# Kernel optimization log

Measured on AMD Instinct MI355X. Metric: run time of the kernel, lower is better.

## Reference

```python
import jax, jax.numpy as jnp
import numpy as np

DIM = 512
NUM_HEADS = 8
HEAD_DIM = DIM // NUM_HEADS
B, S = 2, 2048


def setup_inputs() -> dict:
    key = jax.random.key(0)
    ks = jax.random.split(key, 16)
    scale = 1.0 / np.sqrt(DIM)
    inp = {
        "x": jax.random.normal(ks[0], (B, S, DIM), dtype=jnp.float32),
        "Qexpl": jax.random.normal(ks[1], (B, S, DIM), dtype=jnp.float32),
        "Kexpl": jax.random.normal(ks[2], (B, S, DIM), dtype=jnp.float32),
        "fl": jax.random.uniform(ks[3], (B,), dtype=jnp.float32),
        "fu": jax.random.uniform(ks[4], (B,), dtype=jnp.float32),
        "age": jax.random.uniform(ks[5], (B,), dtype=jnp.float32),
        "gender": jax.random.uniform(ks[6], (B,), dtype=jnp.float32),
        # Linear params: weight stored as [out, in] like torch; y = x @ W.T + b
        "Wq": jax.random.normal(ks[7], (DIM, DIM), dtype=jnp.float32) * scale,
        "bq": jnp.zeros((DIM,), dtype=jnp.float32),
        "Wk": jax.random.normal(ks[8], (DIM, DIM), dtype=jnp.float32) * scale,
        "bk": jnp.zeros((DIM,), dtype=jnp.float32),
        "Wv": jax.random.normal(ks[9], (DIM, DIM), dtype=jnp.float32) * scale,
        "bv": jnp.zeros((DIM,), dtype=jnp.float32),
        "Wo": jax.random.normal(ks[10], (DIM, DIM), dtype=jnp.float32) * scale,
        "bo": jnp.zeros((DIM,), dtype=jnp.float32),
    }
    return inp


def reference(x, Qexpl, Kexpl, fl, fu, age, gender, Wq, bq, Wk, bk, Wv, bv, Wo, bo):
    # drofe_fn is None -> Q/K projections used directly.
    Q = Qexpl @ Wq.T + bq            # [B, S, D]
    K = Kexpl @ Wk.T + bk            # [B, S, D]
    V = x @ Wv.T + bv                # [B, S, D]

    def split_heads(t):  # [B, S, D] -> [B, H, S, hd]
        return t.reshape(B, S, NUM_HEADS, HEAD_DIM).transpose(0, 2, 1, 3)

    Qh, Kh, Vh = split_heads(Q), split_heads(K), split_heads(V)
    scale = 1.0 / np.sqrt(HEAD_DIM).astype(np.float32)
    scores = jnp.einsum("bhqd,bhkd->bhqk", Qh, Kh) * scale  # [B, H, S, S]
    weights = jax.nn.softmax(scores, axis=-1)
    attn = jnp.einsum("bhqk,bhkd->bhqd", weights, Vh)        # [B, H, S, hd]
    attn = attn.transpose(0, 2, 1, 3).reshape(B, S, DIM)
    return attn @ Wo.T + bo
```

## Files before the change

### kernel.cpp

```cpp
#include <hip/hip_runtime.h>
#include <hip/hip_bf16.h>

typedef unsigned short ushort_t;
typedef __attribute__((ext_vector_type(8))) short bf16x8;
typedef __attribute__((ext_vector_type(4))) float f32x4;

__device__ __forceinline__ ushort_t f2bf(float f) {
    union { float f; unsigned u; } v; v.f = f;
    unsigned r = v.u + 0x7FFF + ((v.u >> 16) & 1);
    return (ushort_t)(r >> 16);
}
__device__ __forceinline__ bf16x8 ld8(const ushort_t* p) { return *(const bf16x8*)p; }

__device__ __forceinline__ unsigned cvt2(float x, float y) {
    __hip_bfloat162 h = __float22bfloat162_rn(make_float2(x, y));
    unsigned r; __builtin_memcpy(&r, &h, 4); return r;
}
__device__ __forceinline__ bf16x8 pack8f(float4 a, float4 b) {
    union { unsigned u[4]; bf16x8 v; } o;
    o.u[0] = cvt2(a.x, a.y); o.u[1] = cvt2(a.z, a.w);
    o.u[2] = cvt2(b.x, b.y); o.u[3] = cvt2(b.z, b.w);
    return o.v;
}

__global__ __launch_bounds__(256, 2)
void proj_qkv_kernel(const float* __restrict__ Qe, const float* __restrict__ Ke,
                     const float* __restrict__ x,
                     const float* __restrict__ Wq, const float* __restrict__ Wk,
                     const float* __restrict__ Wv,
                     const float* __restrict__ bq, const float* __restrict__ bk,
                     const float* __restrict__ bv,
                     ushort_t* __restrict__ Qo, ushort_t* __restrict__ Ko,
                     ushort_t* __restrict__ Vt)
{
    __shared__ ushort_t smem[2 * 128 * 72];
    ushort_t* lA = smem;
    ushort_t* lB = smem + 128 * 72;

    const int z = blockIdx.z;
    const float* A = (z == 0) ? Qe : (z == 1) ? Ke : x;
    const float* W = (z == 0) ? Wq : (z == 1) ? Wk : Wv;
    const float* bias = (z == 0) ? bq : (z == 1) ? bk : bv;

    const int m0 = blockIdx.y * 128, n0 = blockIdx.x * 128;
    const int t = threadIdx.x;
    const int lane = t & 63, wave = t >> 6;
    const int wm = (wave & 1) * 64, wn = (wave >> 1) * 64;
    const int fr = lane & 15, quad = lane >> 4;

    f32x4 acc[4][4] = {};
    float4 fa[4][2], fw[4][2];

#pragma unroll
    for (int i = 0; i < 4; ++i) {
        int s = i * 256 + t;
        int r = s >> 3, jp = s & 7;
        const float* pa = A + (size_t)(m0 + r) * 512 + jp * 8;
        fa[i][0] = *(const float4*)pa; fa[i][1] = *(const float4*)(pa + 4);
        const float* pw = W + (size_t)(n0 + r) * 512 + jp * 8;
        fw[i][0] = *(const float4*)pw; fw[i][1] = *(const float4*)(pw + 4);
    }

    for (int kk = 0; kk < 8; ++kk) {
        if (kk) __syncthreads();
#pragma unroll
        for (int i = 0; i < 4; ++i) {
            int s = i * 256 + t;
            int r = s >> 3, jp = s & 7;
            *(bf16x8*)(lA + r * 72 + jp * 8) = pack8f(fa[i][0], fa[i][1]);
            *(bf16x8*)(lB + r * 72 + jp * 8) = pack8f(fw[i][0], fw[i][1]);
        }
        __syncthreads();
        if (kk < 7) {
            int k0 = (kk + 1) * 64;
#pragma unroll
            for (int i = 0; i < 4; ++i) {
                int s = i * 256 + t;
                int r = s >> 3, jp = s & 7;
                const float* pa = A + (size_t)(m0 + r) * 512 + k0 + jp * 8;
                fa[i][0] = *(const float4*)pa; fa[i][1] = *(const float4*)(pa + 4);
                const float* pw = W + (size_t)(n0 + r) * 512 + k0 + jp * 8;
                fw[i][0] = *(const float4*)pw; fw[i][1] = *(const float4*)(pw + 4);
            }
        }

#pragma unroll
        for (int ks = 0; ks < 2; ++ks) {
            bf16x8 af[4], bfrag[4];
#pragma unroll
            for (int mt = 0; mt < 4; ++mt)
                af[mt] = ld8(lA + (wm + mt * 16 + fr) * 72 + (ks * 4 + quad) * 8);
#pragma unroll
            for (int nt = 0; nt < 4; ++nt)
                bfrag[nt] = ld8(lB + (wn + nt * 16 + fr) * 72 + (ks * 4 + quad) * 8);
#pragma unroll
            for (int mt = 0; mt < 4; ++mt)
#pragma unroll
                for (int nt = 0; nt < 4; ++nt)
                    acc[mt][nt] = __builtin_amdgcn_mfma_f32_16x16x32_bf16(
                        af[mt], bfrag[nt], acc[mt][nt], 0, 0, 0);
        }
    }

    const float C1 = 0.125f * 1.44269504088896340736f;
    if (z != 2) {
        ushort_t* dst = (z == 0) ? Qo : Ko;
#pragma unroll
        for (int nt = 0; nt < 4; ++nt) {
            int n = n0 + wn + nt * 16 + fr;
            float bb = bias[n];
#pragma unroll
            for (int mt = 0; mt < 4; ++mt) {
                int mb = m0 + wm + mt * 16 + quad * 4;
                if (z == 0) {
#pragma unroll
                    for (int r = 0; r < 4; ++r)
                        dst[(size_t)(mb + r) * 512 + n] = f2bf((acc[mt][nt][r] + bb) * C1);
                } else {
#pragma unroll
                    for (int r = 0; r < 4; ++r)
                        dst[(size_t)(mb + r) * 512 + n] = f2bf(acc[mt][nt][r] + bb);
                }
            }
        }
    } else {
        __syncthreads();
        ushort_t* lT = smem;
#pragma unroll
        for (int nt = 0; nt < 4; ++nt) {
            int nl = wn + nt * 16 + fr;
            float bb = bias[n0 + nl];
#pragma unroll
            for (int mt = 0; mt < 4; ++mt) {
                int tm = wm + mt * 16 + quad * 4;
#pragma unroll
                for (int r = 0; r < 4; ++r) {
                    int tl = tm + r;
                    int sg = 8 * (tl & 15) + ((tl >> 4) & 7);
                    lT[nl * 136 + sg] = f2bf(acc[mt][nt][r] + bb);
                }
            }
        }
        __syncthreads();
        const int bidx = m0 >> 11, m0t = m0 & 2047;
#pragma unroll
        for (int i = 0; i < 8; ++i) {
            int s = i * 256 + t;
            int row = s >> 4, c = s & 15;
            int n = n0 + row;
            int h = n >> 6, d = n & 63;
            bf16x8 v = ld8(lT + row * 136 + c * 8);
            *(bf16x8*)(Vt + ((size_t)((bidx * 8 + h) * 64 + d)) * 2048 + m0t + c * 8) = v;
        }
    }
}

__global__ __launch_bounds__(256, 2)
void gemm_o_kernel(const ushort_t* __restrict__ A, const float* __restrict__ W,
                   const float* __restrict__ bias, float* __restrict__ dst)
{
    __shared__ ushort_t lA[64 * 72];
    __shared__ ushort_t lB[64 * 72];
    const int m0 = blockIdx.y * 64, n0 = blockIdx.x * 64;
    const int t = threadIdx.x;
    const int lane = t & 63, wave = t >> 6;
    const int wm = (wave & 1) * 32, wn = (wave >> 1) * 32;
    const int fr = lane & 15, quad = lane >> 4;

    f32x4 acc[2][2] = {};
    bf16x8 va[2];
    float4 fw[2][2];

#pragma unroll
    for (int i = 0; i < 2; ++i) {
        int s = i * 256 + t;
        int r = s >> 3, jp = s & 7;
        va[i] = ld8(A + (size_t)(m0 + r) * 512 + jp * 8);
        const float* p = W + (size_t)(n0 + r) * 512 + jp * 8;
        fw[i][0] = *(const float4*)p; fw[i][1] = *(const float4*)(p + 4);
    }

    for (int kk = 0; kk < 8; ++kk) {
        if (kk) __syncthreads();
#pragma unroll
        for (int i = 0; i < 2; ++i) {
            int s = i * 256 + t;
            int r = s >> 3, jp = s & 7;
            *(bf16x8*)(lA + r * 72 + jp * 8) = va[i];
            *(bf16x8*)(lB + r * 72 + jp * 8) = pack8f(fw[i][0], fw[i][1]);
        }
        __syncthreads();
        if (kk < 7) {
            int k0 = (kk + 1) * 64;
#pragma unroll
            for (int i = 0; i < 2; ++i) {
                int s = i * 256 + t;
                int r = s >> 3, jp = s & 7;
                va[i] = ld8(A + (size_t)(m0 + r) * 512 + k0 + jp * 8);
                const float* p = W + (size_t)(n0 + r) * 512 + k0 + jp * 8;
                fw[i][0] = *(const float4*)p; fw[i][1] = *(const float4*)(p + 4);
            }
        }

        bf16x8 af[2][2], bfrag[2][2];
#pragma unroll
        for (int ks = 0; ks < 2; ++ks) {
#pragma unroll
            for (int mt = 0; mt < 2; ++mt)
                af[mt][ks] = ld8(lA + (wm + mt * 16 + fr) * 72 + (ks * 4 + quad) * 8);
#pragma unroll
            for (int nt = 0; nt < 2; ++nt)
                bfrag[nt][ks] = ld8(lB + (wn + nt * 16 + fr) * 72 + (ks * 4 + quad) * 8);
        }
#pragma unroll
        for (int ks = 0; ks < 2; ++ks)
#pragma unroll
            for (int mt = 0; mt < 2; ++mt)
#pragma unroll
                for (int nt = 0; nt < 2; ++nt)
                    acc[mt][nt] = __builtin_amdgcn_mfma_f32_16x16x32_bf16(
                        af[mt][ks], bfrag[nt][ks], acc[mt][nt], 0, 0, 0);
    }

#pragma unroll
    for (int nt = 0; nt < 2; ++nt) {
        int n = n0 + wn + nt * 16 + fr;
        float bb = bias[n];
#pragma unroll
        for (int mt = 0; mt < 2; ++mt) {
            int mb = m0 + wm + mt * 16 + quad * 4;
#pragma unroll
            for (int r = 0; r < 4; ++r)
                dst[(size_t)(mb + r) * 512 + n] = acc[mt][nt][r] + bb;
        }
    }
}

__global__ __launch_bounds__(256, 2)
void attn_kernel(const ushort_t* __restrict__ Q, const ushort_t* __restrict__ K,
                 const ushort_t* __restrict__ Vt, ushort_t* __restrict__ O)
{
    __shared__ ushort_t lK[128 * 72];
    __shared__ ushort_t lVt[64 * 136];
    __shared__ ushort_t lP[64 * 136];

    const int b = blockIdx.z, h = blockIdx.y;
    const int q0 = blockIdx.x * 64;
    const int t = threadIdx.x;
    const int lane = t & 63, wave = t >> 6;
    const int wq = wave * 16;
    const int fr = lane & 15, quad = lane >> 4;

    bf16x8 aq[2];
    {
        const ushort_t* qp = Q + (size_t)(b * 2048 + q0 + wq + fr) * 512 + h * 64 + quad * 8;
        aq[0] = ld8(qp);
        aq[1] = ld8(qp + 32);
    }

    f32x4 oacc[4] = {};
    float lpart[4] = {};
    bf16x8 vk[4], vv[4];

#pragma unroll
    for (int i = 0; i < 4; ++i) {
        int s = i * 256 + t;
        int r = s >> 3, jp = s & 7;
        vk[i] = ld8(K + (size_t)(b * 2048 + r) * 512 + h * 64 + jp * 8);
        int r2 = s >> 4, jp2 = s & 15;
        vv[i] = ld8(Vt + (size_t)((b * 8 + h) * 64 + r2) * 2048 + jp2 * 8);
    }

    for (int kv = 0; kv < 2048; kv += 128) {
        if (kv) __syncthreads();
#pragma unroll
        for (int i = 0; i < 4; ++i) {
            int s = i * 256 + t;
            int r = s >> 3, jp = s & 7;
            *(bf16x8*)(lK + r * 72 + jp * 8) = vk[i];
            int r2 = s >> 4, jp2 = s & 15;
            *(bf16x8*)(lVt + r2 * 136 + jp2 * 8) = vv[i];
        }
        __syncthreads();
        if (kv + 128 < 2048) {
            int kn = kv + 128;
#pragma unroll
            for (int i = 0; i < 4; ++i) {
                int s = i * 256 + t;
                int r = s >> 3, jp = s & 7;
                vk[i] = ld8(K + (size_t)(b * 2048 + kn + r) * 512 + h * 64 + jp * 8);
                int r2 = s >> 4, jp2 = s & 15;
                vv[i] = ld8(Vt + (size_t)((b * 8 + h) * 64 + r2) * 2048 + kn + jp2 * 8);
            }
        }

        f32x4 sc[8] = {};
#pragma unroll
        for (int ks = 0; ks < 2; ++ks)
#pragma unroll
            for (int nt = 0; nt < 8; ++nt) {
                bf16x8 kb = ld8(lK + (nt * 16 + fr) * 72 + (ks * 4 + quad) * 8);
                sc[nt] = __builtin_amdgcn_mfma_f32_16x16x32_bf16(aq[ks], kb, sc[nt], 0, 0, 0);
            }

#pragma unroll
        for (int r = 0; r < 4; ++r) {
            int row = wq + quad * 4 + r;
            float pv[8];
            float acc = 0.f;
#pragma unroll
            for (int nt = 0; nt < 8; ++nt) {
                pv[nt] = exp2f(sc[nt][r]);
                acc += pv[nt];
            }
            lpart[r] += acc;
            union { unsigned u[4]; bf16x8 v; } pu;
            pu.u[0] = cvt2(pv[0], pv[1]); pu.u[1] = cvt2(pv[2], pv[3]);
            pu.u[2] = cvt2(pv[4], pv[5]); pu.u[3] = cvt2(pv[6], pv[7]);
            *(bf16x8*)(lP + row * 136 + fr * 8) = pu.v;
        }

#pragma unroll
        for (int ks = 0; ks < 4; ++ks) {
            bf16x8 ap = ld8(lP + (wq + fr) * 136 + ks * 32 + quad * 8);
#pragma unroll
            for (int nt = 0; nt < 4; ++nt) {
                bf16x8 vb = ld8(lVt + (nt * 16 + fr) * 136 + ks * 32 + quad * 8);
                oacc[nt] = __builtin_amdgcn_mfma_f32_16x16x32_bf16(ap, vb, oacc[nt], 0, 0, 0);
            }
        }
    }

#pragma unroll
    for (int r = 0; r < 4; ++r) {
        float rs = lpart[r];
#pragma unroll
        for (int o = 1; o < 16; o <<= 1)
            rs += __shfl_xor(rs, o, 64);
        float inv = 1.f / rs;
        int q = q0 + wq + quad * 4 + r;
#pragma unroll
        for (int nt = 0; nt < 4; ++nt) {
            int d = nt * 16 + fr;
            O[(size_t)(b * 2048 + q) * 512 + h * 64 + d] = f2bf(oacc[nt][r] * inv);
        }
    }
}

extern "C" void kernel_launch(void* const* d_in, const int* in_sizes, int n_in,
                              void* d_out, int out_size, void* d_ws, size_t ws_size,
                              hipStream_t stream) {
    const float* x   = (const float*)d_in[0];
    const float* Qe  = (const float*)d_in[1];
    const float* Ke  = (const float*)d_in[2];
    const float* Wq  = (const float*)d_in[7];
    const float* bq  = (const float*)d_in[8];
    const float* Wk  = (const float*)d_in[9];
    const float* bk  = (const float*)d_in[10];
    const float* Wv  = (const float*)d_in[11];
    const float* bv  = (const float*)d_in[12];
    const float* Wo  = (const float*)d_in[13];
    const float* bo  = (const float*)d_in[14];

    const size_t NTOK = 2 * 2048;
    const size_t ACT = NTOK * 512;

    ushort_t* p = (ushort_t*)d_ws;
    ushort_t* Qws = p; p += ACT;
    ushort_t* Kws = p; p += ACT;
    ushort_t* Vt  = p; p += ACT;
    ushort_t* Ows = p; p += ACT;

    proj_qkv_kernel<<<dim3(4, 32, 3), 256, 0, stream>>>(Qe, Ke, x, Wq, Wk, Wv,
                                                        bq, bk, bv, Qws, Kws, Vt);
    attn_kernel<<<dim3(32, 8, 2), 256, 0, stream>>>(Qws, Kws, Vt, Ows);
    gemm_o_kernel<<<dim3(8, 64), 256, 0, stream>>>(Ows, Wo, bo, (float*)d_out);
}
```

Before: 167.0 us.

## Restructure attention with direct global-to-LDS loads, double-buffered K, and swizzled LDS

Rewrites the attention kernel to use 2 waves per block, each owning 32 query rows, which doubles register reuse of each K/V fragment across two MFMA tiles. K and V tiles move straight from global memory into LDS with global_load_lds. K is double-buffered so the next tile's load overlaps the current compute. Padded LDS rows are replaced by XOR swizzling to avoid bank conflicts. The cost is fewer waves per block and reliance on manual vmcnt waits, which lowers occupancy and latency hiding.

```diff
diff --git a/kernel.cpp b/kernel.cpp
--- a/kernel.cpp
+++ b/kernel.cpp
@@ -21,6 +21,12 @@
     o.u[0] = cvt2(a.x, a.y); o.u[1] = cvt2(a.z, a.w);
     o.u[2] = cvt2(b.x, b.y); o.u[3] = cvt2(b.z, b.w);
     return o.v;
+}
+
+__device__ __forceinline__ void gload_lds16(const ushort_t* g, ushort_t* l) {
+    __builtin_amdgcn_global_load_lds(
+        (const __attribute__((address_space(1))) void*)g,
+        (__attribute__((address_space(3))) void*)l, 16, 0, 0);
 }
 
 __global__ __launch_bounds__(256, 2)
@@ -236,115 +242,121 @@
     }
 }
 
-__global__ __launch_bounds__(256, 2)
+__global__ __launch_bounds__(128, 1)
 void attn_kernel(const ushort_t* __restrict__ Q, const ushort_t* __restrict__ K,
                  const ushort_t* __restrict__ Vt, ushort_t* __restrict__ O)
 {
-    __shared__ ushort_t lK[128 * 72];
-    __shared__ ushort_t lVt[64 * 136];
-    __shared__ ushort_t lP[64 * 136];
+    __shared__ ushort_t lK[2 * 128 * 64];
+    __shared__ ushort_t lV[64 * 128];
+    __shared__ ushort_t lP[64 * 128];
 
     const int b = blockIdx.z, h = blockIdx.y;
     const int q0 = blockIdx.x * 64;
     const int t = threadIdx.x;
-    const int lane = t & 63, wave = t >> 6;
-    const int wq = wave * 16;
+    const int lane = t & 63, w = t >> 6;
+    const int wq = w * 32;
     const int fr = lane & 15, quad = lane >> 4;
-
-    bf16x8 aq[2];
-    {
-        const ushort_t* qp = Q + (size_t)(b * 2048 + q0 + wq + fr) * 512 + h * 64 + quad * 8;
-        aq[0] = ld8(qp);
-        aq[1] = ld8(qp + 32);
-    }
-
-    f32x4 oacc[4] = {};
-    float lpart[4] = {};
-    bf16x8 vk[4], vv[4];
-
-#pragma unroll
-    for (int i = 0; i < 4; ++i) {
-        int s = i * 256 + t;
-        int r = s >> 3, jp = s & 7;
-        vk[i] = ld8(K + (size_t)(b * 2048 + r) * 512 + h * 64 + jp * 8);
-        int r2 = s >> 4, jp2 = s & 15;
-        vv[i] = ld8(Vt + (size_t)((b * 8 + h) * 64 + r2) * 2048 + jp2 * 8);
-    }
-
-    for (int kv = 0; kv < 2048; kv += 128) {
-        if (kv) __syncthreads();
-#pragma unroll
-        for (int i = 0; i < 4; ++i) {
-            int s = i * 256 + t;
-            int r = s >> 3, jp = s & 7;
-            *(bf16x8*)(lK + r * 72 + jp * 8) = vk[i];
-            int r2 = s >> 4, jp2 = s & 15;
-            *(bf16x8*)(lVt + r2 * 136 + jp2 * 8) = vv[i];
-        }
-        __syncthreads();
-        if (kv + 128 < 2048) {
-            int kn = kv + 128;
-#pragma unroll
-            for (int i = 0; i < 4; ++i) {
-                int s = i * 256 + t;
-                int r = s >> 3, jp = s & 7;
-                vk[i] = ld8(K + (size_t)(b * 2048 + kn + r) * 512 + h * 64 + jp * 8);
-                int r2 = s >> 4, jp2 = s & 15;
-                vv[i] = ld8(Vt + (size_t)((b * 8 + h) * 64 + r2) * 2048 + kn + jp2 * 8);
-            }
-        }
-
-        f32x4 sc[8] = {};
+    const int fr7 = fr & 7;
+
+    bf16x8 aq[2][2];
+#pragma unroll
+    for (int mq = 0; mq < 2; ++mq) {
+        const ushort_t* qp = Q + (size_t)(b * 2048 + q0 + wq + mq * 16 + fr) * 512
+                               + h * 64 + quad * 8;
+        aq[mq][0] = ld8(qp);
+        aq[mq][1] = ld8(qp + 32);
+    }
+
+    const int krow = w * 8 + (lane >> 3);
+    const ushort_t* kbase = K + (size_t)(b * 2048 + krow) * 512 + h * 64
+                              + (((lane & 7) ^ (krow & 7)) << 3);
+    const int vrow = w * 4 + (lane >> 4);
+    const ushort_t* vbase = Vt + (size_t)((b * 8 + h) * 64 + vrow) * 2048
+                              + (((lane & 15) ^ (vrow & 7)) << 3);
+
+#pragma unroll
+    for (int i = 0; i < 8; ++i)
+        gload_lds16(kbase + (size_t)(i * 16) * 512, lK + (i * 16 + w * 8) * 64);
+    __syncthreads();
+
+    f32x4 oacc[2][4] = {};
+    float lpart[2][4] = {};
+
+    for (int tt = 0; tt < 16; ++tt) {
+        const int kv = tt << 7;
+        ushort_t* lKc = lK + ((tt & 1) << 13);
+        ushort_t* lKn = lK + (((tt & 1) ^ 1) << 13);
+
+#pragma unroll
+        for (int i = 0; i < 8; ++i)
+            gload_lds16(vbase + kv + (size_t)(i * 8) * 2048, lV + (i * 8 + w * 4) * 128);
+        if (tt < 15) {
+#pragma unroll
+            for (int i = 0; i < 8; ++i)
+                gload_lds16(kbase + (size_t)(kv + 128 + i * 16) * 512,
+                            lKn + (i * 16 + w * 8) * 64);
+        }
+
+        f32x4 sc[2][8] = {};
 #pragma unroll
         for (int ks = 0; ks < 2; ++ks)
 #pragma unroll
             for (int nt = 0; nt < 8; ++nt) {
-                bf16x8 kb = ld8(lK + (nt * 16 + fr) * 72 + (ks * 4 + quad) * 8);
-                sc[nt] = __builtin_amdgcn_mfma_f32_16x16x32_bf16(aq[ks], kb, sc[nt], 0, 0, 0);
-            }
-
+                bf16x8 kb = ld8(lKc + (nt * 16 + fr) * 64 + (((ks * 4 + quad) ^ fr7) << 3));
+                sc[0][nt] = __builtin_amdgcn_mfma_f32_16x16x32_bf16(aq[0][ks], kb, sc[0][nt], 0, 0, 0);
+                sc[1][nt] = __builtin_amdgcn_mfma_f32_16x16x32_bf16(aq[1][ks], kb, sc[1][nt], 0, 0, 0);
+            }
+
+#pragma unroll
+        for (int mq = 0; mq < 2; ++mq)
+#pragma unroll
+            for (int r = 0; r < 4; ++r) {
+                int row = wq + mq * 16 + quad * 4 + r;
+                float pv[8]; float acc = 0.f;
+#pragma unroll
+                for (int nt = 0; nt < 8; ++nt) { pv[nt] = exp2f(sc[mq][nt][r]); acc += pv[nt]; }
+                lpart[mq][r] += acc;
+                union { unsigned u[4]; bf16x8 v; } pu;
+                pu.u[0] = cvt2(pv[0], pv[1]); pu.u[1] = cvt2(pv[2], pv[3]);
+                pu.u[2] = cvt2(pv[4], pv[5]); pu.u[3] = cvt2(pv[6], pv[7]);
+                *(bf16x8*)(lP + row * 128 + ((fr ^ (row & 7)) << 3)) = pu.v;
+            }
+
+        if (tt < 15) asm volatile("s_waitcnt vmcnt(8)" ::: "memory");
+        else         asm volatile("s_waitcnt vmcnt(0)" ::: "memory");
+        __builtin_amdgcn_s_barrier();
+        __builtin_amdgcn_sched_barrier(0);
+
+#pragma unroll
+        for (int ks = 0; ks < 4; ++ks) {
+            int cs = ((ks * 4 + quad) ^ fr7) << 3;
+            bf16x8 ap0 = ld8(lP + (wq + fr) * 128 + cs);
+            bf16x8 ap1 = ld8(lP + (wq + 16 + fr) * 128 + cs);
+#pragma unroll
+            for (int nt = 0; nt < 4; ++nt) {
+                bf16x8 vb = ld8(lV + (nt * 16 + fr) * 128 + cs);
+                oacc[0][nt] = __builtin_amdgcn_mfma_f32_16x16x32_bf16(ap0, vb, oacc[0][nt], 0, 0, 0);
+                oacc[1][nt] = __builtin_amdgcn_mfma_f32_16x16x32_bf16(ap1, vb, oacc[1][nt], 0, 0, 0);
+            }
+        }
+        __syncthreads();
+    }
+
+#pragma unroll
+    for (int mq = 0; mq < 2; ++mq)
 #pragma unroll
         for (int r = 0; r < 4; ++r) {
-            int row = wq + quad * 4 + r;
-            float pv[8];
-            float acc = 0.f;
-#pragma unroll
-            for (int nt = 0; nt < 8; ++nt) {
-                pv[nt] = exp2f(sc[nt][r]);
-                acc += pv[nt];
-            }
-            lpart[r] += acc;
-            union { unsigned u[4]; bf16x8 v; } pu;
-            pu.u[0] = cvt2(pv[0], pv[1]); pu.u[1] = cvt2(pv[2], pv[3]);
-            pu.u[2] = cvt2(pv[4], pv[5]); pu.u[3] = cvt2(pv[6], pv[7]);
-            *(bf16x8*)(lP + row * 136 + fr * 8) = pu.v;
-        }
-
-#pragma unroll
-        for (int ks = 0; ks < 4; ++ks) {
-            bf16x8 ap = ld8(lP + (wq + fr) * 136 + ks * 32 + quad * 8);
-#pragma unroll
-            for (int nt = 0; nt < 4; ++nt) {
-                bf16x8 vb = ld8(lVt + (nt * 16 + fr) * 136 + ks * 32 + quad * 8);
-                oacc[nt] = __builtin_amdgcn_mfma_f32_16x16x32_bf16(ap, vb, oacc[nt], 0, 0, 0);
-            }
-        }
-    }
-
-#pragma unroll
-    for (int r = 0; r < 4; ++r) {
-        float rs = lpart[r];
-#pragma unroll
-        for (int o = 1; o < 16; o <<= 1)
-            rs += __shfl_xor(rs, o, 64);
-        float inv = 1.f / rs;
-        int q = q0 + wq + quad * 4 + r;
-#pragma unroll
-        for (int nt = 0; nt < 4; ++nt) {
-            int d = nt * 16 + fr;
-            O[(size_t)(b * 2048 + q) * 512 + h * 64 + d] = f2bf(oacc[nt][r] * inv);
-        }
-    }
+            float rs = lpart[mq][r];
+#pragma unroll
+            for (int o = 1; o < 16; o <<= 1)
+                rs += __shfl_xor(rs, o, 64);
+            float inv = 1.f / rs;
+            int q = q0 + wq + mq * 16 + quad * 4 + r;
+#pragma unroll
+            for (int nt = 0; nt < 4; ++nt)
+                O[(size_t)(b * 2048 + q) * 512 + h * 64 + nt * 16 + fr] =
+                    f2bf(oacc[mq][nt][r] * inv);
+        }
 }
 
 extern "C" void kernel_launch(void* const* d_in, const int* in_sizes, int n_in,
@@ -373,6 +385,6 @@
 
     proj_qkv_kernel<<<dim3(4, 32, 3), 256, 0, stream>>>(Qe, Ke, x, Wq, Wk, Wv,
                                                         bq, bk, bv, Qws, Kws, Vt);
-    attn_kernel<<<dim3(32, 8, 2), 256, 0, stream>>>(Qws, Kws, Vt, Ows);
+    attn_kernel<<<dim3(32, 8, 2), 128, 0, stream>>>(Qws, Kws, Vt, Ows);
     gemm_o_kernel<<<dim3(8, 64), 256, 0, stream>>>(Ows, Wo, bo, (float*)d_out);
 }
```

After: 181.2 us. 8.5% more time.

## Stream K/V tiles directly into LDS with async loads and XOR swizzle

Applied to the files above, without the earlier changes.

Replaces the register-staged K/V prefetch in the attention kernel with global_load_lds direct-to-LDS loads. K is double-buffered and prefetched one tile ahead, while V is loaded per tile and overlaps the QK^T and softmax work. Padded LDS rows are replaced by XOR-swizzled unpadded layouts for K, V and P to avoid bank conflicts, and explicit vmcnt waits plus barriers order the loads. This removes register pressure and VGPR-to-LDS store traffic, but relies on correct manual waitcnt accounting and adds a per-tile V load latency that is only partly hidden.

```diff
diff --git a/kernel.cpp b/kernel.cpp
--- a/kernel.cpp
+++ b/kernel.cpp
@@ -21,6 +21,12 @@
     o.u[0] = cvt2(a.x, a.y); o.u[1] = cvt2(a.z, a.w);
     o.u[2] = cvt2(b.x, b.y); o.u[3] = cvt2(b.z, b.w);
     return o.v;
+}
+
+__device__ __forceinline__ void gload_lds16(const ushort_t* g, ushort_t* l) {
+    __builtin_amdgcn_global_load_lds(
+        (const __attribute__((address_space(1))) void*)g,
+        (__attribute__((address_space(3))) void*)l, 16, 0, 0);
 }
 
 __global__ __launch_bounds__(256, 2)
@@ -240,16 +246,17 @@
 void attn_kernel(const ushort_t* __restrict__ Q, const ushort_t* __restrict__ K,
                  const ushort_t* __restrict__ Vt, ushort_t* __restrict__ O)
 {
-    __shared__ ushort_t lK[128 * 72];
-    __shared__ ushort_t lVt[64 * 136];
-    __shared__ ushort_t lP[64 * 136];
+    __shared__ ushort_t lK[2 * 128 * 64];
+    __shared__ ushort_t lV[64 * 128];
+    __shared__ ushort_t lP[64 * 128];
 
     const int b = blockIdx.z, h = blockIdx.y;
     const int q0 = blockIdx.x * 64;
     const int t = threadIdx.x;
-    const int lane = t & 63, wave = t >> 6;
-    const int wq = wave * 16;
+    const int lane = t & 63, w = t >> 6;
+    const int wq = w * 16;
     const int fr = lane & 15, quad = lane >> 4;
+    const int fr7 = fr & 7;
 
     bf16x8 aq[2];
     {
@@ -258,40 +265,34 @@
         aq[1] = ld8(qp + 32);
     }
 
+    const int krl = lane >> 3;
+    const ushort_t* kbase = K + (size_t)(b * 2048 + w * 32 + krl) * 512 + h * 64
+                              + (((lane & 7) ^ (krl & 7)) << 3);
+    const int vrl = w * 4 + (lane >> 4);
+    const ushort_t* vbase = Vt + (size_t)((b * 8 + h) * 64 + vrl) * 2048
+                              + (((lane & 15) ^ (vrl & 7)) << 3);
+
+#pragma unroll
+    for (int i = 0; i < 4; ++i)
+        gload_lds16(kbase + (size_t)(i * 8) * 512, lK + (w * 32 + i * 8) * 64);
+    __syncthreads();
+
     f32x4 oacc[4] = {};
     float lpart[4] = {};
-    bf16x8 vk[4], vv[4];
-
-#pragma unroll
-    for (int i = 0; i < 4; ++i) {
-        int s = i * 256 + t;
-        int r = s >> 3, jp = s & 7;
-        vk[i] = ld8(K + (size_t)(b * 2048 + r) * 512 + h * 64 + jp * 8);
-        int r2 = s >> 4, jp2 = s & 15;
-        vv[i] = ld8(Vt + (size_t)((b * 8 + h) * 64 + r2) * 2048 + jp2 * 8);
-    }
-
-    for (int kv = 0; kv < 2048; kv += 128) {
-        if (kv) __syncthreads();
-#pragma unroll
-        for (int i = 0; i < 4; ++i) {
-            int s = i * 256 + t;
-            int r = s >> 3, jp = s & 7;
-            *(bf16x8*)(lK + r * 72 + jp * 8) = vk[i];
-            int r2 = s >> 4, jp2 = s & 15;
-            *(bf16x8*)(lVt + r2 * 136 + jp2 * 8) = vv[i];
-        }
-        __syncthreads();
-        if (kv + 128 < 2048) {
-            int kn = kv + 128;
-#pragma unroll
-            for (int i = 0; i < 4; ++i) {
-                int s = i * 256 + t;
-                int r = s >> 3, jp = s & 7;
-                vk[i] = ld8(K + (size_t)(b * 2048 + kn + r) * 512 + h * 64 + jp * 8);
-                int r2 = s >> 4, jp2 = s & 15;
-                vv[i] = ld8(Vt + (size_t)((b * 8 + h) * 64 + r2) * 2048 + kn + jp2 * 8);
-            }
+
+    for (int tt = 0; tt < 16; ++tt) {
+        const int kv = tt << 7;
+        ushort_t* lKc = lK + ((tt & 1) << 13);
+        ushort_t* lKn = lK + (((tt & 1) ^ 1) << 13);
+
+#pragma unroll
+        for (int i = 0; i < 4; ++i)
+            gload_lds16(vbase + kv + (size_t)(i * 16) * 2048, lV + (i * 16 + w * 4) * 128);
+        if (tt < 15) {
+#pragma unroll
+            for (int i = 0; i < 4; ++i)
+                gload_lds16(kbase + (size_t)(kv + 128 + i * 8) * 512,
+                            lKn + (w * 32 + i * 8) * 64);
         }
 
         f32x4 sc[8] = {};
@@ -299,36 +300,39 @@
         for (int ks = 0; ks < 2; ++ks)
 #pragma unroll
             for (int nt = 0; nt < 8; ++nt) {
-                bf16x8 kb = ld8(lK + (nt * 16 + fr) * 72 + (ks * 4 + quad) * 8);
+                bf16x8 kb = ld8(lKc + (nt * 16 + fr) * 64 + (((ks * 4 + quad) ^ fr7) << 3));
                 sc[nt] = __builtin_amdgcn_mfma_f32_16x16x32_bf16(aq[ks], kb, sc[nt], 0, 0, 0);
             }
 
 #pragma unroll
         for (int r = 0; r < 4; ++r) {
             int row = wq + quad * 4 + r;
-            float pv[8];
-            float acc = 0.f;
-#pragma unroll
-            for (int nt = 0; nt < 8; ++nt) {
-                pv[nt] = exp2f(sc[nt][r]);
-                acc += pv[nt];
-            }
+            float pv[8]; float acc = 0.f;
+#pragma unroll
+            for (int nt = 0; nt < 8; ++nt) { pv[nt] = exp2f(sc[nt][r]); acc += pv[nt]; }
             lpart[r] += acc;
             union { unsigned u[4]; bf16x8 v; } pu;
             pu.u[0] = cvt2(pv[0], pv[1]); pu.u[1] = cvt2(pv[2], pv[3]);
             pu.u[2] = cvt2(pv[4], pv[5]); pu.u[3] = cvt2(pv[6], pv[7]);
-            *(bf16x8*)(lP + row * 136 + fr * 8) = pu.v;
-        }
+            *(bf16x8*)(lP + row * 128 + ((fr ^ (row & 7)) << 3)) = pu.v;
+        }
+
+        if (tt < 15) asm volatile("s_waitcnt vmcnt(4)" ::: "memory");
+        else         asm volatile("s_waitcnt vmcnt(0)" ::: "memory");
+        __builtin_amdgcn_s_barrier();
+        __builtin_amdgcn_sched_barrier(0);
 
 #pragma unroll
         for (int ks = 0; ks < 4; ++ks) {
-            bf16x8 ap = ld8(lP + (wq + fr) * 136 + ks * 32 + quad * 8);
+            int cs = ((ks * 4 + quad) ^ fr7) << 3;
+            bf16x8 ap = ld8(lP + (wq + fr) * 128 + cs);
 #pragma unroll
             for (int nt = 0; nt < 4; ++nt) {
-                bf16x8 vb = ld8(lVt + (nt * 16 + fr) * 136 + ks * 32 + quad * 8);
+                bf16x8 vb = ld8(lV + (nt * 16 + fr) * 128 + cs);
                 oacc[nt] = __builtin_amdgcn_mfma_f32_16x16x32_bf16(ap, vb, oacc[nt], 0, 0, 0);
             }
         }
+        __syncthreads();
     }
 
 #pragma unroll
```

Result: no change. 165.3 us (-1.0%).
